# Optimization experiments

Hardware: AMD Instinct MI355X
Metric: run time of the kernel (lower is better)

## Reference

```python
import jax, jax.numpy as jnp
import numpy as np

B, IN, H, NB = 8192, 1024, 2048, 8
BS = H // NB  # 256


def setup_inputs() -> dict:
    key = jax.random.key(0)
    ks = jax.random.split(key, 4)
    s = 0.02
    return {
        "x": jax.random.normal(ks[0], (B, IN), dtype=jnp.float32),
        "h": jax.random.normal(ks[1], (B, H), dtype=jnp.float32),
        "W_ir": jax.random.normal(ks[2], (3 * H, IN), dtype=jnp.float32) * s,
        "b_ir_lin": jnp.zeros((3 * H,), dtype=jnp.float32),
        "b_ir": jnp.zeros((3 * H,), dtype=jnp.float32),
        "W_h": jax.random.normal(ks[3], (NB, 3 * BS, BS), dtype=jnp.float32) * s,
        "b_hr": jnp.zeros((3 * H,), dtype=jnp.float32),
    }


def reference(x, h, W_ir, b_ir_lin, b_ir, W_h, b_hr):
    b = x.shape[0]
    nb, three_bs, bs = W_h.shape
    hdim = nb * bs
    # input projection: w_ir(x) + b_ir  -> [B, 3H], chunked globally into r,z,n
    wx = x @ W_ir.T + b_ir_lin + b_ir
    wxr, wxz, wxn = jnp.split(wx, 3, axis=1)
    wxr = wxr.reshape(b, nb, bs)
    wxz = wxz.reshape(b, nb, bs)
    wxn = wxn.reshape(b, nb, bs)
    # block-diagonal hidden projection: per-block Linear(bs -> 3*bs), no bias
    hb = h.reshape(b, nb, bs)
    # b_hr is sliced in contiguous chunks of 3*bs per block (local r,z,n layout)
    wh = jnp.einsum('bki,koi->bko', hb, W_h) + b_hr.reshape(nb, three_bs)
    whr, whz, whn = jnp.split(wh, 3, axis=2)
    r = jax.nn.sigmoid(wxr + whr)
    z = jax.nn.sigmoid(wxz + whz)
    n = jnp.tanh(wxn + r * whn)
    h_new = (1.0 - z) * hb + z * n
    return h_new.reshape(b, hdim)
```

## Files before the change

### kernel.cpp

```cpp
#include <hip/hip_runtime.h>
#include <cstdint>
#include <cstddef>


typedef __attribute__((ext_vector_type(8))) short bf16x8;
typedef __attribute__((ext_vector_type(4))) float f32x4;

__device__ __forceinline__ unsigned short f2bf(float f) {
    uint32_t u = __float_as_uint(f);
    u += 0x7FFFu + ((u >> 16) & 1u);
    return (unsigned short)(u >> 16);
}
__device__ __forceinline__ float bf2f(unsigned short b) {
    return __uint_as_float(((uint32_t)b) << 16);
}

__device__ __forceinline__ void gload16(const void* g, void* l) {
    __builtin_amdgcn_global_load_lds(
        (const __attribute__((address_space(1))) void*)g,
        (__attribute__((address_space(3))) void*)l,
        16, 0, 0);
}

__device__ __forceinline__ float sigmoidf_(float x) {
    return 1.0f / (1.0f + __expf(-x));
}
__device__ __forceinline__ float tanhf_(float x) {
    float e = __expf(-2.0f * fabsf(x));
    float t = (1.0f - e) / (1.0f + e);
    return copysignf(t, x);
}

__global__ __launch_bounds__(256)
void cast_all(const float* __restrict__ x, const float* __restrict__ wir,
              const float* __restrict__ h, const float* __restrict__ wh,
              unsigned short* __restrict__ xb, unsigned short* __restrict__ wirb,
              unsigned short* __restrict__ hb, unsigned short* __restrict__ whb) {
    const int i = blockIdx.x * 256 + threadIdx.x;
    const float* s; unsigned short* d; int j;
    if (i < 2097152)      { s = x;   d = xb;   j = i; }
    else if (i < 3670016) { s = wir; d = wirb; j = i - 2097152; }
    else if (i < 7864320) { s = h;   d = hb;   j = i - 3670016; }
    else                  { s = wh;  d = whb;  j = i - 7864320; }
    const float4 v = *reinterpret_cast<const float4*>(s + (size_t)j * 4);
    ushort4 o;
    o.x = f2bf(v.x); o.y = f2bf(v.y); o.z = f2bf(v.z); o.w = f2bf(v.w);
    *reinterpret_cast<ushort4*>(d + (size_t)j * 4) = o;
}


#define MFMA24(NT) do {                                                        \
    asm volatile("s_waitcnt lgkmcnt(0)" ::: "memory");                         \
    __builtin_amdgcn_sched_barrier(0);                                         \
    __builtin_amdgcn_s_setprio(1);                                             \
    _Pragma("unroll")                                                          \
    for (int m_ = 0; m_ < 4; ++m_) {                                           \
        acc[0][m_][0] = __builtin_amdgcn_mfma_f32_16x16x32_bf16(               \
            av[m_], bv[0][0], acc[0][m_][0], 0, 0, 0);                         \
        acc[0][m_][1] = __builtin_amdgcn_mfma_f32_16x16x32_bf16(               \
            av[m_], bv[0][1], acc[0][m_][1], 0, 0, 0);                         \
        acc[1][m_][0] = __builtin_amdgcn_mfma_f32_16x16x32_bf16(               \
            av[m_], bv[1][0], acc[1][m_][0], 0, 0, 0);                         \
        acc[1][m_][1] = __builtin_amdgcn_mfma_f32_16x16x32_bf16(               \
            av[m_], bv[1][1], acc[1][m_][1], 0, 0, 0);                         \
        acc[NT][m_][0] = __builtin_amdgcn_mfma_f32_16x16x32_bf16(              \
            av[m_], bv[2][0], acc[NT][m_][0], 0, 0, 0);                        \
        acc[NT][m_][1] = __builtin_amdgcn_mfma_f32_16x16x32_bf16(              \
            av[m_], bv[2][1], acc[NT][m_][1], 0, 0, 0);                        \
    }                                                                          \
    __builtin_amdgcn_s_setprio(0);                                             \
} while (0)

#define LDA(m, kb_) (*(const bf16x8*)(aS + (wm * 64 + (m) * 16 + fr) * 64 + (kb_)))
#define LDB(s, n_, kb_) (*(const bf16x8*)(bS + ((s) * 64 + wn * 32 + (n_) * 16 + fr) * 64 + (kb_)))

#define I0_1(kt, ds) do {                                                      \
    gload16(b1[0] + (size_t)(kt) * 64, Bs + (ds) * 12288 + 0 * 2048 + doff);   \
    gload16(b1[1] + (size_t)(kt) * 64, Bs + (ds) * 12288 + 1 * 2048 + doff);   \
    gload16(b1[2] + (size_t)(kt) * 64, Bs + (ds) * 12288 + 2 * 2048 + doff);   \
    gload16(b1[3] + (size_t)(kt) * 64, Bs + (ds) * 12288 + 3 * 2048 + doff); } while (0)
#define I1_1(kt, ds) do {                                                      \
    gload16(b1[4] + (size_t)(kt) * 64, Bs + (ds) * 12288 + 4 * 2048 + doff);   \
    gload16(b1[5] + (size_t)(kt) * 64, Bs + (ds) * 12288 + 5 * 2048 + doff);   \
    gload16(a1[0] + (size_t)(kt) * 64, As + (ds) * 8192 + 0 * 2048 + doff);    \
    gload16(a1[1] + (size_t)(kt) * 64, As + (ds) * 8192 + 1 * 2048 + doff); } while (0)
#define I2_1(kt, ds) do {                                                      \
    gload16(a1[2] + (size_t)(kt) * 64, As + (ds) * 8192 + 2 * 2048 + doff);    \
    gload16(a1[3] + (size_t)(kt) * 64, As + (ds) * 8192 + 3 * 2048 + doff); } while (0)
#define I0_2(k2, ds) do {                                                      \
    gload16(b2[0] + (size_t)(k2) * 64, Bs + (ds) * 12288 + 0 * 2048 + doff);   \
    gload16(b2[1] + (size_t)(k2) * 64, Bs + (ds) * 12288 + 1 * 2048 + doff);   \
    gload16(b2[2] + (size_t)(k2) * 64, Bs + (ds) * 12288 + 2 * 2048 + doff);   \
    gload16(b2[3] + (size_t)(k2) * 64, Bs + (ds) * 12288 + 3 * 2048 + doff); } while (0)
#define I1_2(k2, ds) do {                                                      \
    gload16(b2[4] + (size_t)(k2) * 64, Bs + (ds) * 12288 + 4 * 2048 + doff);   \
    gload16(b2[5] + (size_t)(k2) * 64, Bs + (ds) * 12288 + 5 * 2048 + doff);   \
    gload16(a2[0] + (size_t)(k2) * 64, As + (ds) * 8192 + 0 * 2048 + doff);    \
    gload16(a2[1] + (size_t)(k2) * 64, As + (ds) * 8192 + 1 * 2048 + doff); } while (0)
#define I2_2(k2, ds) do {                                                      \
    gload16(a2[2] + (size_t)(k2) * 64, As + (ds) * 8192 + 2 * 2048 + doff);    \
    gload16(a2[3] + (size_t)(k2) * 64, As + (ds) * 8192 + 3 * 2048 + doff); } while (0)

#define KSTEP(slot_, I0, W0, I1, I2, NT) do {                                  \
    const unsigned short* aS = As + (slot_) * 8192;                            \
    const unsigned short* bS = Bs + (slot_) * 12288;                           \
    I0;                                                                        \
    asm volatile("s_waitcnt vmcnt(" W0 ")" ::: "memory");                      \
    __builtin_amdgcn_s_barrier();                                              \
    _Pragma("unroll") for (int m_ = 0; m_ < 4; ++m_) av[m_] = LDA(m_, kb0);    \
    _Pragma("unroll") for (int s_ = 0; s_ < 3; ++s_) {                         \
        bv[s_][0] = LDB(s_, 0, kb0); bv[s_][1] = LDB(s_, 1, kb0); }            \
    I1;                                                                        \
    __builtin_amdgcn_s_barrier();                                              \
    MFMA24(NT);                                                                \
    __builtin_amdgcn_s_barrier();                                              \
    _Pragma("unroll") for (int m_ = 0; m_ < 4; ++m_) av[m_] = LDA(m_, kb1);    \
    _Pragma("unroll") for (int s_ = 0; s_ < 3; ++s_) {                         \
        bv[s_][0] = LDB(s_, 0, kb1); bv[s_][1] = LDB(s_, 1, kb1); }            \
    I2;                                                                        \
    __builtin_amdgcn_s_barrier();                                              \
    MFMA24(NT);                                                                \
    __builtin_amdgcn_s_barrier();                                              \
} while (0)

__global__ __launch_bounds__(256, 2)
void gru_fused(const unsigned short* __restrict__ Xb,
               const unsigned short* __restrict__ Wirb,
               const unsigned short* __restrict__ Hbb,
               const unsigned short* __restrict__ Whb,
               const float* __restrict__ b_ir_lin,
               const float* __restrict__ b_ir,
               const float* __restrict__ b_hr,
               float* __restrict__ out) {
    constexpr int K1 = 1024, H = 2048;
    __shared__ unsigned short lds[2 * 8192 + 2 * 12288];
    unsigned short* const As = lds;
    unsigned short* const Bs = lds + 2 * 8192;

    const int tid  = threadIdx.x;
    const int lane = tid & 63;
    const int w    = tid >> 6;
    const int wm   = w >> 1;
    const int wn   = w & 1;

    const int bid  = blockIdx.x;
    const int kb   = bid & 7;
    const int idx  = bid >> 3;
    const int bm   = (idx >> 2) * 128;
    const int hsub = idx & 3;
    const int hcb  = kb * 256 + hsub * 64;

    const int srow  = tid >> 3;
    const int chunk = (tid & 7) ^ (srow & 7);
    const int scol  = chunk * 8;
    const int doff  = tid * 8;
    const unsigned short* a1[4];
    const unsigned short* a2[4];
    #pragma unroll
    for (int q = 0; q < 4; ++q) {
        a1[q] = Xb  + (size_t)(bm + q * 32 + srow) * K1 + scol;
        a2[q] = Hbb + (size_t)(bm + q * 32 + srow) * H + kb * 256 + scol;
    }
    const unsigned short* b1[6];
    const unsigned short* b2[6];
    #pragma unroll
    for (int q = 0; q < 6; ++q) {
        const int s  = q >> 1;
        const int rr = (q & 1) * 32 + srow;
        b1[q] = Wirb + (size_t)(s * 2048 + hcb + rr) * K1 + scol;
        b2[q] = Whb + (size_t)kb * 196608 + (size_t)(s * 256 + hsub * 64 + rr) * 256 + scol;
    }

    const int fr  = lane & 15;
    const int k0e = (lane >> 4) * 8;
    const int mfr = (fr & 7) << 4;
    const int kb0 = ((k0e * 2) ^ mfr) >> 1;
    const int kb1 = (((k0e * 2) + 64) ^ mfr) >> 1;

    f32x4 acc[4][4][2] = {};
    bf16x8 av[4], bv[3][2];

    I0_1(0, 0); I1_1(0, 0); I2_1(0, 0);

    #pragma unroll 1
    for (int t = 0; t < 15; ++t) {
        const int sl = t & 1, nx = sl ^ 1;
        KSTEP(sl, I0_1(t + 1, nx), "4", I1_1(t + 1, nx), I2_1(t + 1, nx), 2);
    }
    KSTEP(1, I0_2(0, 0), "4", I1_2(0, 0), I2_2(0, 0), 2);
    #pragma unroll 1
    for (int t = 16; t < 19; ++t) {
        const int sl = t & 1, nx = sl ^ 1;
        KSTEP(sl, I0_2(t - 15, nx), "4", I1_2(t - 15, nx), I2_2(t - 15, nx), 3);
    }
    KSTEP(1, ((void)0), "0", ((void)0), ((void)0), 3);

    const int rq = (lane >> 4) * 4;
    #pragma unroll
    for (int n = 0; n < 2; ++n) {
        const int hcol = hcb + wn * 32 + n * 16 + fr;
        const int lcol = hcol & 255;
        const float bir0 = b_ir_lin[hcol]        + b_ir[hcol];
        const float bir1 = b_ir_lin[2048 + hcol] + b_ir[2048 + hcol];
        const float bir2 = b_ir_lin[4096 + hcol] + b_ir[4096 + hcol];
        const float bhr0 = b_hr[kb * 768 + lcol];
        const float bhr1 = b_hr[kb * 768 + 256 + lcol];
        const float bhr2 = b_hr[kb * 768 + 512 + lcol];
        #pragma unroll
        for (int mi = 0; mi < 4; ++mi) {
            #pragma unroll
            for (int r = 0; r < 4; ++r) {
                const int row = bm + wm * 64 + mi * 16 + rq + r;
                const float pr = acc[0][mi][n][r] + bir0 + bhr0;
                const float pz = acc[1][mi][n][r] + bir1 + bhr1;
                const float xn = acc[2][mi][n][r] + bir2;
                const float hn = acc[3][mi][n][r] + bhr2;
                const float rg = sigmoidf_(pr);
                const float zg = sigmoidf_(pz);
                const float ng = tanhf_(xn + rg * hn);
                const float hv = bf2f(Hbb[(size_t)row * H + hcol]);
                out[(size_t)row * H + hcol] = (1.0f - zg) * hv + zg * ng;
            }
        }
    }
}

extern "C" void kernel_launch(void* const* d_in, const int* in_sizes, int n_in,
                              void* d_out, int out_size, void* d_ws, size_t ws_size,
                              hipStream_t stream) {
    const float* x        = (const float*)d_in[0];
    const float* h        = (const float*)d_in[1];
    const float* W_ir     = (const float*)d_in[2];
    const float* b_ir_lin = (const float*)d_in[3];
    const float* b_ir     = (const float*)d_in[4];
    const float* W_h      = (const float*)d_in[5];
    const float* b_hr     = (const float*)d_in[6];
    float* out = (float*)d_out;

    char* ws = (char*)d_ws;
    unsigned short* xb   = (unsigned short*)(ws);
    unsigned short* wirb = (unsigned short*)(ws + 16777216);
    unsigned short* hb   = (unsigned short*)(ws + 29360128);
    unsigned short* whb  = (unsigned short*)(ws + 62914560);

    cast_all<<<32256, 256, 0, stream>>>(x, W_ir, h, W_h, xb, wirb, hb, whb);

    gru_fused<<<2048, 256, 0, stream>>>(xb, wirb, hb, whb,
                                        b_ir_lin, b_ir, b_hr, out);
}
```

Before: 170.6 us.

## Simplify K-loop pipeline to one barrier per step with bulk prefetch

New measurement: 170.3 us. No clear change (-0.1%).

```diff
diff --git a/kernel.cpp b/kernel.cpp
--- a/kernel.cpp
+++ b/kernel.cpp
@@ -50,9 +50,6 @@
 
 
 #define MFMA24(NT) do {                                                        \
-    asm volatile("s_waitcnt lgkmcnt(0)" ::: "memory");                         \
-    __builtin_amdgcn_sched_barrier(0);                                         \
-    __builtin_amdgcn_s_setprio(1);                                             \
     _Pragma("unroll")                                                          \
     for (int m_ = 0; m_ < 4; ++m_) {                                           \
         acc[0][m_][0] = __builtin_amdgcn_mfma_f32_16x16x32_bf16(               \
@@ -68,59 +65,48 @@
         acc[NT][m_][1] = __builtin_amdgcn_mfma_f32_16x16x32_bf16(              \
             av[m_], bv[2][1], acc[NT][m_][1], 0, 0, 0);                        \
     }                                                                          \
-    __builtin_amdgcn_s_setprio(0);                                             \
 } while (0)
 
 #define LDA(m, kb_) (*(const bf16x8*)(aS + (wm * 64 + (m) * 16 + fr) * 64 + (kb_)))
 #define LDB(s, n_, kb_) (*(const bf16x8*)(bS + ((s) * 64 + wn * 32 + (n_) * 16 + fr) * 64 + (kb_)))
 
-#define I0_1(kt, ds) do {                                                      \
+#define I_1(kt, ds) do {                                                       \
     gload16(b1[0] + (size_t)(kt) * 64, Bs + (ds) * 12288 + 0 * 2048 + doff);   \
     gload16(b1[1] + (size_t)(kt) * 64, Bs + (ds) * 12288 + 1 * 2048 + doff);   \
     gload16(b1[2] + (size_t)(kt) * 64, Bs + (ds) * 12288 + 2 * 2048 + doff);   \
-    gload16(b1[3] + (size_t)(kt) * 64, Bs + (ds) * 12288 + 3 * 2048 + doff); } while (0)
-#define I1_1(kt, ds) do {                                                      \
+    gload16(b1[3] + (size_t)(kt) * 64, Bs + (ds) * 12288 + 3 * 2048 + doff);   \
     gload16(b1[4] + (size_t)(kt) * 64, Bs + (ds) * 12288 + 4 * 2048 + doff);   \
     gload16(b1[5] + (size_t)(kt) * 64, Bs + (ds) * 12288 + 5 * 2048 + doff);   \
     gload16(a1[0] + (size_t)(kt) * 64, As + (ds) * 8192 + 0 * 2048 + doff);    \
-    gload16(a1[1] + (size_t)(kt) * 64, As + (ds) * 8192 + 1 * 2048 + doff); } while (0)
-#define I2_1(kt, ds) do {                                                      \
+    gload16(a1[1] + (size_t)(kt) * 64, As + (ds) * 8192 + 1 * 2048 + doff);    \
     gload16(a1[2] + (size_t)(kt) * 64, As + (ds) * 8192 + 2 * 2048 + doff);    \
     gload16(a1[3] + (size_t)(kt) * 64, As + (ds) * 8192 + 3 * 2048 + doff); } while (0)
-#define I0_2(k2, ds) do {                                                      \
+#define I_2(k2, ds) do {                                                       \
     gload16(b2[0] + (size_t)(k2) * 64, Bs + (ds) * 12288 + 0 * 2048 + doff);   \
     gload16(b2[1] + (size_t)(k2) * 64, Bs + (ds) * 12288 + 1 * 2048 + doff);   \
     gload16(b2[2] + (size_t)(k2) * 64, Bs + (ds) * 12288 + 2 * 2048 + doff);   \
-    gload16(b2[3] + (size_t)(k2) * 64, Bs + (ds) * 12288 + 3 * 2048 + doff); } while (0)
-#define I1_2(k2, ds) do {                                                      \
+    gload16(b2[3] + (size_t)(k2) * 64, Bs + (ds) * 12288 + 3 * 2048 + doff);   \
     gload16(b2[4] + (size_t)(k2) * 64, Bs + (ds) * 12288 + 4 * 2048 + doff);   \
     gload16(b2[5] + (size_t)(k2) * 64, Bs + (ds) * 12288 + 5 * 2048 + doff);   \
     gload16(a2[0] + (size_t)(k2) * 64, As + (ds) * 8192 + 0 * 2048 + doff);    \
-    gload16(a2[1] + (size_t)(k2) * 64, As + (ds) * 8192 + 1 * 2048 + doff); } while (0)
-#define I2_2(k2, ds) do {                                                      \
+    gload16(a2[1] + (size_t)(k2) * 64, As + (ds) * 8192 + 1 * 2048 + doff);    \
     gload16(a2[2] + (size_t)(k2) * 64, As + (ds) * 8192 + 2 * 2048 + doff);    \
     gload16(a2[3] + (size_t)(k2) * 64, As + (ds) * 8192 + 3 * 2048 + doff); } while (0)
 
-#define KSTEP(slot_, I0, W0, I1, I2, NT) do {                                  \
+#define KSTEP(slot_, ISSUE, NT) do {                                           \
+    asm volatile("s_waitcnt vmcnt(0)" ::: "memory");                           \
+    __builtin_amdgcn_s_barrier();                                              \
+    ISSUE;                                                                     \
     const unsigned short* aS = As + (slot_) * 8192;                            \
     const unsigned short* bS = Bs + (slot_) * 12288;                           \
-    I0;                                                                        \
-    asm volatile("s_waitcnt vmcnt(" W0 ")" ::: "memory");                      \
-    __builtin_amdgcn_s_barrier();                                              \
     _Pragma("unroll") for (int m_ = 0; m_ < 4; ++m_) av[m_] = LDA(m_, kb0);    \
     _Pragma("unroll") for (int s_ = 0; s_ < 3; ++s_) {                         \
         bv[s_][0] = LDB(s_, 0, kb0); bv[s_][1] = LDB(s_, 1, kb0); }            \
-    I1;                                                                        \
-    __builtin_amdgcn_s_barrier();                                              \
     MFMA24(NT);                                                                \
-    __builtin_amdgcn_s_barrier();                                              \
     _Pragma("unroll") for (int m_ = 0; m_ < 4; ++m_) av[m_] = LDA(m_, kb1);    \
     _Pragma("unroll") for (int s_ = 0; s_ < 3; ++s_) {                         \
         bv[s_][0] = LDB(s_, 0, kb1); bv[s_][1] = LDB(s_, 1, kb1); }            \
-    I2;                                                                        \
-    __builtin_amdgcn_s_barrier();                                              \
     MFMA24(NT);                                                                \
-    __builtin_amdgcn_s_barrier();                                              \
 } while (0)
 
 __global__ __launch_bounds__(256, 2)
@@ -180,20 +166,20 @@
     f32x4 acc[4][4][2] = {};
     bf16x8 av[4], bv[3][2];
 
-    I0_1(0, 0); I1_1(0, 0); I2_1(0, 0);
+    I_1(0, 0);
 
     #pragma unroll 1
     for (int t = 0; t < 15; ++t) {
         const int sl = t & 1, nx = sl ^ 1;
-        KSTEP(sl, I0_1(t + 1, nx), "4", I1_1(t + 1, nx), I2_1(t + 1, nx), 2);
-    }
-    KSTEP(1, I0_2(0, 0), "4", I1_2(0, 0), I2_2(0, 0), 2);
+        KSTEP(sl, I_1(t + 1, nx), 2);
+    }
+    KSTEP(1, I_2(0, 0), 2);
     #pragma unroll 1
     for (int t = 16; t < 19; ++t) {
         const int sl = t & 1, nx = sl ^ 1;
-        KSTEP(sl, I0_2(t - 15, nx), "4", I1_2(t - 15, nx), I2_2(t - 15, nx), 3);
-    }
-    KSTEP(1, ((void)0), "0", ((void)0), ((void)0), 3);
+        KSTEP(sl, I_2(t - 15, nx), 3);
+    }
+    KSTEP(1, ((void)0), 3);
 
     const int rq = (lane >> 4) * 4;
     #pragma unroll
```
